# Optimization experiments

Measured on AMD Instinct MI355X. Metric: run time of the kernel, lower is better.

Reference implementation:

```python
import jax, jax.numpy as jnp
import numpy as np

# Fixed geometry from the module's voxel_dict
VOXEL = np.array([0.32, 0.32, 6.0], dtype=np.float32)
PC_MIN = np.array([-74.88, -74.88, -2.0], dtype=np.float32)
PC_MAX = np.array([74.88, 74.88, 4.0], dtype=np.float32)
NX, NY, NZ = 468, 468, 1          # round((max-min)/voxel) per axis
CANVAS = NZ * NY * NX             # 219024 voxels (batch_size = 1)
OFFSET = VOXEL / 2.0 + PC_MIN     # x/y/z_offset from __init__


def setup_inputs() -> dict:
    key = jax.random.key(0)
    k1, k2, k3, k4 = jax.random.split(key, 4)
    N = 400000
    # points uniformly inside the point-cloud range (dynamic voxelization keeps all)
    xyz = jax.random.uniform(k1, (N, 3), dtype=jnp.float32) * (PC_MAX - PC_MIN) * 0.999 + PC_MIN
    extra = jax.random.normal(k2, (N, 2), dtype=jnp.float32)
    points = jnp.concatenate([xyz, extra], axis=1)          # [N, 5]
    W1 = jax.random.normal(k3, (11, 64), dtype=jnp.float32) * 0.05
    W2 = jax.random.normal(k4, (128, 64), dtype=jnp.float32) * 0.05
    return {"points": points, "W1": W1, "W2": W2}


def _flat_voxel_index(xyz):
    # dynamic voxelization: integer voxel coord per point, (z, y, x) ordering
    c = jnp.floor((xyz - PC_MIN) / VOXEL).astype(jnp.int32)
    cx = jnp.clip(c[:, 0], 0, NX - 1)
    cy = jnp.clip(c[:, 1], 0, NY - 1)
    cz = jnp.clip(c[:, 2], 0, NZ - 1)
    flat = cz * (NY * NX) + cy * NX + cx                    # canvas index as in map_voxel_center_to_point
    return flat, cx, cy, cz


def reference(points, W1, W2):
    xyz = points[:, :3]
    flat, cx, cy, cz = _flat_voxel_index(xyz)

    # DynamicScatter mean (cluster_scatter)
    cnt = jax.ops.segment_sum(jnp.ones((points.shape[0],), jnp.float32), flat, num_segments=CANVAS)
    vsum = jax.ops.segment_sum(points, flat, num_segments=CANVAS)
    vmean = vsum / jnp.maximum(cnt, 1.0)[:, None]           # [CANVAS, 5]
    pmean = vmean[flat]                                     # gather voxel mean to points

    f_cluster = xyz - pmean[:, :3]
    centers = jnp.stack([cx, cy, cz], axis=1).astype(jnp.float32) * VOXEL + OFFSET
    f_center = xyz - centers
    features = jnp.concatenate([points, f_cluster, f_center], axis=-1)   # [N, 11]

    occ = (cnt > 0)[:, None]

    # PFN layer 1: Linear(bias=False) + ReLU, then scatter-max to voxels
    pf1 = jax.nn.relu(features @ W1)                        # [N, 64]
    v1 = jax.ops.segment_max(pf1, flat, num_segments=CANVAS)
    v1 = jnp.where(occ, v1, 0.0)                            # zero empty voxels (replaces -inf)

    # gather voxel max back to points, concat, PFN layer 2
    feat2 = jnp.concatenate([pf1, v1[flat]], axis=1)        # [N, 128]
    pf2 = jax.nn.relu(feat2 @ W2)                           # [N, 64]
    v2 = jax.ops.segment_max(pf2, flat, num_segments=CANVAS)
    v2 = jnp.where(occ, v2, 0.0)                            # [CANVAS, 64] dense voxel features
    return v2
```

## Files before the change

kernel.cpp:

```cpp
#include <hip/hip_runtime.h>

#define NXc 468
#define NYc 468
#define CANVASc (468 * 468)
#define NPTS 400000
#define RUN 16
#define NRUNS (NPTS / RUN)
#define GPTS ((NPTS + 255) / 256)
#define GVOX ((CANVASc + 255) / 256)
#define GSEAM ((NRUNS + 255) / 256)

#define PCMIN_X (-74.88f)
#define PCMIN_Y (-74.88f)
#define VOX_X 0.32f
#define VOX_Y 0.32f
#define OFF_X (-74.72f)
#define OFF_Y (-74.72f)
#define OFF_Z (1.0f)

typedef __attribute__((ext_vector_type(8))) short v8s;
typedef __attribute__((ext_vector_type(4))) float v4f;

static_assert(sizeof(__bf16) == 2, "bf16 must be 2 bytes");

__device__ __forceinline__ int rli(int x, int p) {
    return __builtin_amdgcn_readlane(x, p);
}

__device__ __forceinline__ void split8(const float* f, v8s& h, v8s& l) {
    #pragma unroll
    for (int i = 0; i < 8; i += 2) {
        __bf16 h0 = (__bf16)f[i];
        __bf16 h1 = (__bf16)f[i + 1];
        h[i]     = __builtin_bit_cast(short, h0);
        h[i + 1] = __builtin_bit_cast(short, h1);
        float l0 = f[i]     - (float)h0;
        float l1 = f[i + 1] - (float)h1;
        l[i]     = __builtin_bit_cast(short, (__bf16)l0);
        l[i + 1] = __builtin_bit_cast(short, (__bf16)l1);
    }
}

__device__ __forceinline__ int voxel_cell(float x, float y, int& cx, int& cy) {
    cx = (int)floorf((x - PCMIN_X) / VOX_X);
    cy = (int)floorf((y - PCMIN_Y) / VOX_Y);
    cx = min(max(cx, 0), NXc - 1);
    cy = min(max(cy, 0), NYc - 1);
    return cy * NXc + cx;
}

__device__ __forceinline__ void kw_body(int tid,
                                        const float* __restrict__ W1,
                                        const float* __restrict__ W2,
                                        v8s* __restrict__ w1frag,
                                        v8s* __restrict__ w2frag) {
    if (tid < 1024) {
        int f = tid >> 6, lane = tid & 63;
        int t = f >> 2, c = f & 3;
        int q = lane >> 4, n = lane & 15;
        float v[8];
        #pragma unroll
        for (int i = 0; i < 8; i++) v[i] = W2[(c * 32 + q * 8 + i) * 64 + t * 16 + n];
        v8s h, l;
        split8(v, h, l);
        w2frag[(f * 2 + 0) * 64 + lane] = h;
        w2frag[(f * 2 + 1) * 64 + lane] = l;
    } else if (tid < 1280) {
        int f = (tid - 1024) >> 6, lane = (tid - 1024) & 63;
        int q = lane >> 4, n = lane & 15;
        float v[8];
        #pragma unroll
        for (int i = 0; i < 8; i++) {
            int k = q * 8 + i;
            v[i] = (k < 11) ? W1[k * 64 + f * 16 + n] : 0.f;
        }
        v8s h, l;
        split8(v, h, l);
        w1frag[(f * 2 + 0) * 64 + lane] = h;
        w1frag[(f * 2 + 1) * 64 + lane] = l;
    }
}

__global__ __launch_bounds__(256) void k_stats(const float* __restrict__ pts,
                                               int* __restrict__ cnt,
                                               const float* __restrict__ W1,
                                               const float* __restrict__ W2,
                                               v8s* __restrict__ w1frag,
                                               v8s* __restrict__ w2frag) {
    int b = blockIdx.x;
    if (b >= GPTS) {
        kw_body((b - GPTS) * 256 + threadIdx.x, W1, W2, w1frag, w2frag);
        return;
    }
    int i = b * 256 + threadIdx.x;
    if (i >= NPTS) return;
    float x = pts[i * 5 + 0], y = pts[i * 5 + 1];
    int cx, cy;
    int fl = voxel_cell(x, y, cx, cy);
    atomicAdd(&cnt[fl], 1);
}

__global__ __launch_bounds__(256) void k_alloc(const int* __restrict__ cnt,
                                               int* __restrict__ cursor,
                                               int* __restrict__ gcur) {
    int v = blockIdx.x * 256 + threadIdx.x;
    int lane = threadIdx.x & 63;
    int c = (v < CANVASc) ? cnt[v] : 0;
    int scan = c;
    #pragma unroll
    for (int off = 1; off < 64; off <<= 1) {
        int t = __shfl_up(scan, off, 64);
        if (lane >= off) scan += t;
    }
    int total = __shfl(scan, 63, 64);
    int base = 0;
    if (lane == 0 && total > 0) base = atomicAdd(gcur, total);
    base = __shfl(base, 0, 64);
    if (v < CANVASc) cursor[v] = base + scan - c;
}

__device__ __forceinline__ void gather_pt(const float* __restrict__ pts, int pi,
                                          float4& A, float& e1) {
    const float* pp = pts + (size_t)pi * 5;
    __builtin_memcpy(&A, pp, 16);
    e1 = pp[4];
}

__global__ __launch_bounds__(256) void k_scatter(const float* __restrict__ pts,
                                                 int* __restrict__ cursor,
                                                 float4* __restrict__ pos4,
                                                 float* __restrict__ e1b,
                                                 int* __restrict__ cellb) {
    int i = blockIdx.x * 256 + threadIdx.x;
    if (i >= NPTS) return;
    float4 A; float e1;
    gather_pt(pts, i, A, e1);
    int cx, cy;
    int fl = voxel_cell(A.x, A.y, cx, cy);
    int pos = atomicAdd(&cursor[fl], 1);
    pos4[pos] = A;
    e1b[pos] = e1;
    cellb[pos] = cx | (cy << 16);
}

__global__ __launch_bounds__(256) void kV(const int* __restrict__ cnt,
                                          const int* __restrict__ cursor,
                                          const float4* __restrict__ pos4,
                                          const int* __restrict__ cellb,
                                          float4* __restrict__ vmean4,
                                          float4* __restrict__ v14,
                                          float4* __restrict__ out4) {
    int b = blockIdx.x;
    if (b >= GVOX) {
        int w = (b - GVOX) * 256 + threadIdx.x;
        if (w == 0 || w >= NRUNS) return;
        int bb = w * RUN;
        int ca = cellb[bb - 1], cb = cellb[bb];
        if (ca != cb) return;
        int cx = ca & 0xFFFF, cy = ca >> 16;
        int va = cy * NXc + cx;
        float4 z = make_float4(0.f, 0.f, 0.f, 0.f);
        float4* o = out4 + (size_t)va * 16;
        float4* q = v14 + (size_t)va * 16;
        #pragma unroll
        for (int i = 0; i < 16; i++) { o[i] = z; q[i] = z; }
        return;
    }
    int v = b * 256 + threadIdx.x;
    if (v >= CANVASc) return;
    int c = cnt[v];
    if (c == 0) {
        float4 z = make_float4(0.f, 0.f, 0.f, 0.f);
        float4* o = out4 + (size_t)v * 16;
        #pragma unroll
        for (int i = 0; i < 16; i++) o[i] = z;
        return;
    }
    int start = cursor[v] - c;
    float sx = 0.f, sy = 0.f, sz = 0.f;
    for (int i = 0; i < c; i++) {
        float4 p = pos4[start + i];
        sx += p.x; sy += p.y; sz += p.z;
    }
    float inv = 1.0f / (float)c;
    vmean4[v] = make_float4(sx * inv, sy * inv, sz * inv, 0.f);
}

struct PtRegs {
    float4 A;
    float  e1, fcx, fcy, fcz;
    float  mx, my, mz;
    int    vx;
};
__device__ __forceinline__ PtRegs load_pt(const float4* __restrict__ pos4,
                                          const float* __restrict__ e1b,
                                          const int* __restrict__ cellb,
                                          const float4* __restrict__ vmean4,
                                          int base, int j) {
    PtRegs r;
    r.A = make_float4(0.f, 0.f, 0.f, 0.f);
    r.e1 = r.fcx = r.fcy = r.fcz = r.mx = r.my = r.mz = 0.f;
    r.vx = -1;
    int idx = -1;
    if (j < RUN) idx = base + j;
    else if (j == 16) idx = (base + RUN < NPTS) ? base + RUN : -1;
    else if (j == 17) idx = base - 1;
    if (idx >= 0) {
        int cell = cellb[idx];
        int cx = cell & 0xFFFF, cy = cell >> 16;
        int vv = cy * NXc + cx;
        r.vx = vv;
        if (j < RUN) {
            float4 A = pos4[idx];
            r.A = A;
            r.e1 = e1b[idx];
            r.fcx = A.x - (cx * VOX_X + OFF_X);
            r.fcy = A.y - (cy * VOX_Y + OFF_Y);
            r.fcz = A.z - OFF_Z;
            float4 m = vmean4[vv];
            r.mx = m.x; r.my = m.y; r.mz = m.z;
        }
    }
    return r;
}

#define PSTR 68

__device__ __forceinline__ void phase1_mfma(float (*s_pf)[PSTR], const PtRegs& P,
                                            const v8s* __restrict__ w1frag, int j) {
    if (j < RUN) {
        float* row = s_pf[j];
        row[0] = P.A.x; row[1] = P.A.y; row[2] = P.A.z; row[3] = P.A.w; row[4] = P.e1;
        row[5] = P.A.x - P.mx; row[6] = P.A.y - P.my; row[7] = P.A.z - P.mz;
        row[8] = P.fcx; row[9] = P.fcy; row[10] = P.fcz;
        #pragma unroll
        for (int t = 11; t < 16; t++) row[t] = 0.f;
    }
    __builtin_amdgcn_wave_barrier();

    const int m = j & 15, q = j >> 4;
    v8s fh = {0,0,0,0,0,0,0,0}, fl_ = {0,0,0,0,0,0,0,0};
    if (q < 2) {
        float f8[8];
        #pragma unroll
        for (int i = 0; i < 8; i++) f8[i] = s_pf[m][q * 8 + i];
        split8(f8, fh, fl_);
    }
    v4f d[4];
    #pragma unroll
    for (int t = 0; t < 4; t++) {
        v8s bh = w1frag[(t * 2 + 0) * 64 + j];
        v8s bl = w1frag[(t * 2 + 1) * 64 + j];
        v4f acc = {0.f, 0.f, 0.f, 0.f};
        acc = __builtin_amdgcn_mfma_f32_16x16x32_bf16(fh,  bh, acc, 0, 0, 0);
        acc = __builtin_amdgcn_mfma_f32_16x16x32_bf16(fl_, bh, acc, 0, 0, 0);
        acc = __builtin_amdgcn_mfma_f32_16x16x32_bf16(fh,  bl, acc, 0, 0, 0);
        d[t] = acc;
    }
    __builtin_amdgcn_wave_barrier();
    #pragma unroll
    for (int t = 0; t < 4; t++)
        #pragma unroll
        for (int r = 0; r < 4; r++)
            s_pf[q * 4 + r][t * 16 + m] = fmaxf(d[t][r], 0.f);
    __builtin_amdgcn_wave_barrier();
}

__global__ __launch_bounds__(256) void kA(const float4* __restrict__ pos4,
                                          const float* __restrict__ e1b,
                                          const int* __restrict__ cellb,
                                          const float4* __restrict__ vmean4,
                                          const v8s* __restrict__ w1frag,
                                          float* __restrict__ v1) {
    __shared__ float s_pf[4][RUN][PSTR];
    int wslot = threadIdx.x >> 6;
    int wave = blockIdx.x * 4 + wslot;
    int j = threadIdx.x & 63;
    int base = wave * RUN;

    PtRegs P = load_pt(pos4, e1b, cellb, vmean4, base, j);

    const int first = rli(P.vx, 0), last = rli(P.vx, RUN - 1);
    const bool firstExt = (rli(P.vx, 17) == first);
    const bool lastExt  = (rli(P.vx, 16) == last);
    if (!firstExt && !lastExt) return;

    phase1_mfma(s_pf[wslot], P, w1frag, j);

    int vprev = first;
    float smax = 0.f;
    for (int p = 0; p < RUN; p++) {
        int vp = rli(P.vx, p);
        if (vp != vprev) {
            bool ua = (vprev == first && firstExt) || (vprev == last && lastExt);
            if (ua) atomicMax((int*)v1 + (size_t)vprev * 64 + j, __float_as_int(smax));
            vprev = vp; smax = 0.f;
        }
        smax = fmaxf(smax, s_pf[wslot][p][j]);
    }
    {
        bool ua = (vprev == first && firstExt) || (vprev == last && lastExt);
        if (ua) atomicMax((int*)v1 + (size_t)vprev * 64 + j, __float_as_int(smax));
    }
}

__global__ __launch_bounds__(256) void kB(const float4* __restrict__ pos4,
                                          const float* __restrict__ e1b,
                                          const int* __restrict__ cellb,
                                          const float4* __restrict__ vmean4,
                                          const v8s* __restrict__ w1frag,
                                          const v8s* __restrict__ w2frag,
                                          const float* __restrict__ v1,
                                          float* __restrict__ out) {
    __shared__ float s_pf[4][RUN][PSTR];
    int wslot = threadIdx.x >> 6;
    int wave = blockIdx.x * 4 + wslot;
    int j = threadIdx.x & 63;
    int base = wave * RUN;

    PtRegs P = load_pt(pos4, e1b, cellb, vmean4, base, j);

    const int m = j & 15, q = j >> 4;

    const int first = rli(P.vx, 0), last = rli(P.vx, RUN - 1);
    const bool firstExt = (rli(P.vx, 17) == first);
    const bool lastExt  = (rli(P.vx, 16) == last);

    int vx_m = __builtin_amdgcn_ds_bpermute(m << 2, P.vx);
    int vx_prev = __shfl_up(P.vx, 1, 64);
    unsigned long long B =
        __ballot((j < RUN) && ((j == 0) || (P.vx != vx_prev)));
    int s_seg = 63 - __builtin_clzll(B & ((2ULL << m) - 1ULL));
    int e_seg = m + 1 + (int)__builtin_ctzll((B | (1ULL << RUN)) >> (m + 1));
    const bool ext_m = (vx_m == first && firstExt) || (vx_m == last && lastExt);

    phase1_mfma(s_pf[wslot], P, w1frag, j);

    float vf[16];
    if (ext_m) {
        const float* vr = v1 + (size_t)vx_m * 64 + q * 8;
        #pragma unroll
        for (int c = 0; c < 2; c++)
            #pragma unroll
            for (int i = 0; i < 8; i++) vf[c * 8 + i] = vr[c * 32 + i];
    }

    v8s ah[4], al[4];
    #pragma unroll
    for (int c = 0; c < 2; c++) {
        float f[8];
        #pragma unroll
        for (int i = 0; i < 8; i++) f[i] = s_pf[wslot][m][c * 32 + q * 8 + i];
        split8(f, ah[c], al[c]);
    }
    if (!ext_m) {
        #pragma unroll
        for (int i = 0; i < 16; i++) vf[i] = 0.f;
        for (int p = s_seg; p < e_seg; p++) {
            const float* row = s_pf[wslot][p];
            float4 a0 = *(const float4*)&row[q * 8];
            float4 a1 = *(const float4*)&row[q * 8 + 4];
            float4 b0 = *(const float4*)&row[32 + q * 8];
            float4 b1 = *(const float4*)&row[32 + q * 8 + 4];
            vf[0] = fmaxf(vf[0], a0.x);  vf[1] = fmaxf(vf[1], a0.y);
            vf[2] = fmaxf(vf[2], a0.z);  vf[3] = fmaxf(vf[3], a0.w);
            vf[4] = fmaxf(vf[4], a1.x);  vf[5] = fmaxf(vf[5], a1.y);
            vf[6] = fmaxf(vf[6], a1.z);  vf[7] = fmaxf(vf[7], a1.w);
            vf[8] = fmaxf(vf[8], b0.x);  vf[9] = fmaxf(vf[9], b0.y);
            vf[10] = fmaxf(vf[10], b0.z); vf[11] = fmaxf(vf[11], b0.w);
            vf[12] = fmaxf(vf[12], b1.x); vf[13] = fmaxf(vf[13], b1.y);
            vf[14] = fmaxf(vf[14], b1.z); vf[15] = fmaxf(vf[15], b1.w);
        }
    }
    split8(vf + 0, ah[2], al[2]);
    split8(vf + 8, ah[3], al[3]);
    __builtin_amdgcn_wave_barrier();

    #pragma unroll
    for (int t = 0; t < 4; t++) {
        v8s bh[4], bl[4];
        #pragma unroll
        for (int c = 0; c < 4; c++) {
            bh[c] = w2frag[((t * 4 + c) * 2 + 0) * 64 + j];
            bl[c] = w2frag[((t * 4 + c) * 2 + 1) * 64 + j];
        }
        v4f acc = {0.f, 0.f, 0.f, 0.f};
        #pragma unroll
        for (int c = 0; c < 4; c++) {
            acc = __builtin_amdgcn_mfma_f32_16x16x32_bf16(ah[c], bh[c], acc, 0, 0, 0);
            acc = __builtin_amdgcn_mfma_f32_16x16x32_bf16(al[c], bh[c], acc, 0, 0, 0);
            acc = __builtin_amdgcn_mfma_f32_16x16x32_bf16(ah[c], bl[c], acc, 0, 0, 0);
        }
        #pragma unroll
        for (int r = 0; r < 4; r++) s_pf[wslot][q * 4 + r][t * 16 + m] = acc[r];
    }
    __builtin_amdgcn_wave_barrier();

    int vprev = first;
    float smax = -3.4e38f;
    for (int p = 0; p < RUN; p++) {
        int vp = rli(P.vx, p);
        if (vp != vprev) {
            float r = fmaxf(smax, 0.f);
            size_t o = (size_t)vprev * 64 + j;
            bool ua = (vprev == first && firstExt) || (vprev == last && lastExt);
            if (ua) atomicMax((int*)out + o, __float_as_int(r));
            else out[o] = r;
            vprev = vp; smax = -3.4e38f;
        }
        smax = fmaxf(smax, s_pf[wslot][p][j]);
    }
    {
        float r = fmaxf(smax, 0.f);
        size_t o = (size_t)vprev * 64 + j;
        bool ua = (vprev == first && firstExt) || (vprev == last && lastExt);
        if (ua) atomicMax((int*)out + o, __float_as_int(r));
        else out[o] = r;
    }
}

extern "C" void kernel_launch(void* const* d_in, const int* in_sizes, int n_in,
                              void* d_out, int out_size, void* d_ws, size_t ws_size,
                              hipStream_t stream) {
    const float* pts = (const float*)d_in[0];
    const float* W1  = (const float*)d_in[1];
    const float* W2  = (const float*)d_in[2];
    float* out = (float*)d_out;

    float4* vmean4 = (float4*)d_ws;
    float*  v1     = (float*)(vmean4 + CANVASc);
    float4* pos4   = (float4*)(v1 + (size_t)CANVASc * 64);
    float*  e1b    = (float*)(pos4 + NPTS);
    int*    cellb  = (int*)(e1b + NPTS);
    v8s*    w2frag = (v8s*)(cellb + NPTS);
    v8s*    w1frag = w2frag + 2048;
    int*    cnt    = (int*)(w1frag + 512);
    int*    gcur   = cnt + CANVASc;
    int*    cursor = gcur + 1;

    hipMemsetAsync(cnt, 0, (size_t)(CANVASc + 1) * 4, stream);

    k_stats  <<<GPTS + 5, 256, 0, stream>>>(pts, cnt, W1, W2, w1frag, w2frag);
    k_alloc  <<<GVOX, 256, 0, stream>>>(cnt, cursor, gcur);
    k_scatter<<<GPTS, 256, 0, stream>>>(pts, cursor, pos4, e1b, cellb);
    kV       <<<GVOX + GSEAM, 256, 0, stream>>>(cnt, cursor, pos4, cellb,
                                                vmean4, (float4*)v1, (float4*)out);
    kA       <<<NRUNS / 4, 256, 0, stream>>>(pos4, e1b, cellb, vmean4, w1frag, v1);
    kB       <<<NRUNS / 4, 256, 0, stream>>>(pos4, e1b, cellb, vmean4, w1frag,
                                             w2frag, v1, out);
}
```

Measured before the change: 236.6 us.

## Replace full-run kA pass with seam-voxel list and direct per-voxel max kernel

kA launched one wave per run of 16 points across all runs, recomputed phase-1 features with MFMA and used atomicMax for voxels spanning run boundaries. Now kV records seam voxels into a compacted list, and a new kAL kernel with a fixed grid walks only those voxels. For each one it computes the layer-1 max directly with scalar FMAs over the voxel's points and writes it without atomics. This removes the zeroing of v1 for seam voxels, the atomics and the wasted waves that exited early. In exchange it adds a global atomic counter and uses fp32 FMAs instead of the split-bf16 MFMA, which can change rounding slightly.

```diff
diff --git a/kernel.cpp b/kernel.cpp
--- a/kernel.cpp
+++ b/kernel.cpp
@@ -25,6 +25,9 @@
 
 __device__ __forceinline__ int rli(int x, int p) {
     return __builtin_amdgcn_readlane(x, p);
+}
+__device__ __forceinline__ float rlf(float x, int p) {
+    return __int_as_float(__builtin_amdgcn_readlane(__float_as_int(x), p));
 }
 
 __device__ __forceinline__ void split8(const float* f, v8s& h, v8s& l) {
@@ -148,8 +151,9 @@
                                           const float4* __restrict__ pos4,
                                           const int* __restrict__ cellb,
                                           float4* __restrict__ vmean4,
-                                          float4* __restrict__ v14,
-                                          float4* __restrict__ out4) {
+                                          float4* __restrict__ out4,
+                                          int* __restrict__ scnt,
+                                          int* __restrict__ slist) {
     int b = blockIdx.x;
     if (b >= GVOX) {
         int w = (b - GVOX) * 256 + threadIdx.x;
@@ -159,11 +163,12 @@
         if (ca != cb) return;
         int cx = ca & 0xFFFF, cy = ca >> 16;
         int va = cy * NXc + cx;
+        int pos = atomicAdd(scnt, 1);
+        slist[pos] = va;
         float4 z = make_float4(0.f, 0.f, 0.f, 0.f);
         float4* o = out4 + (size_t)va * 16;
-        float4* q = v14 + (size_t)va * 16;
-        #pragma unroll
-        for (int i = 0; i < 16; i++) { o[i] = z; q[i] = z; }
+        #pragma unroll
+        for (int i = 0; i < 16; i++) o[i] = z;
         return;
     }
     int v = b * 256 + threadIdx.x;
@@ -184,6 +189,57 @@
     }
     float inv = 1.0f / (float)c;
     vmean4[v] = make_float4(sx * inv, sy * inv, sz * inv, 0.f);
+}
+
+__global__ __launch_bounds__(256) void kAL(const int* __restrict__ scnt,
+                                           const int* __restrict__ slist,
+                                           const int* __restrict__ cnt,
+                                           const int* __restrict__ cursor,
+                                           const float4* __restrict__ pos4,
+                                           const float* __restrict__ e1b,
+                                           const int* __restrict__ cellb,
+                                           const float4* __restrict__ vmean4,
+                                           const float* __restrict__ W1,
+                                           float* __restrict__ v1) {
+    int j = threadIdx.x & 63;
+    int wslot = threadIdx.x >> 6;
+    int nseam = scnt[0];
+    float w[11];
+    #pragma unroll
+    for (int k = 0; k < 11; k++) w[k] = W1[k * 64 + j];
+    for (int s = blockIdx.x * 4 + wslot; s < nseam; s += gridDim.x * 4) {
+        int v = slist[s];
+        int c = cnt[v];
+        int start = cursor[v] - c;
+        float vmax = 0.f;
+        for (int pb = 0; pb < c; pb += 64) {
+            int pc = min(c - pb, 64);
+            float f[11];
+            #pragma unroll
+            for (int k = 0; k < 11; k++) f[k] = 0.f;
+            if (j < pc) {
+                int idx = start + pb + j;
+                float4 A = pos4[idx];
+                float e1 = e1b[idx];
+                int cell = cellb[idx];
+                int cx = cell & 0xFFFF, cy = cell >> 16;
+                float4 mv = vmean4[v];
+                f[0] = A.x; f[1] = A.y; f[2] = A.z; f[3] = A.w; f[4] = e1;
+                f[5] = A.x - mv.x; f[6] = A.y - mv.y; f[7] = A.z - mv.z;
+                f[8] = A.x - (cx * VOX_X + OFF_X);
+                f[9] = A.y - (cy * VOX_Y + OFF_Y);
+                f[10] = A.z - OFF_Z;
+            }
+            for (int p = 0; p < pc; p++) {
+                float acc = 0.f;
+                #pragma unroll
+                for (int k = 0; k < 11; k++)
+                    acc = fmaf(rlf(f[k], p), w[k], acc);
+                vmax = fmaxf(vmax, acc);
+            }
+        }
+        v1[(size_t)v * 64 + j] = vmax;
+    }
 }
 
 struct PtRegs {
@@ -266,44 +322,6 @@
     __builtin_amdgcn_wave_barrier();
 }
 
-__global__ __launch_bounds__(256) void kA(const float4* __restrict__ pos4,
-                                          const float* __restrict__ e1b,
-                                          const int* __restrict__ cellb,
-                                          const float4* __restrict__ vmean4,
-                                          const v8s* __restrict__ w1frag,
-                                          float* __restrict__ v1) {
-    __shared__ float s_pf[4][RUN][PSTR];
-    int wslot = threadIdx.x >> 6;
-    int wave = blockIdx.x * 4 + wslot;
-    int j = threadIdx.x & 63;
-    int base = wave * RUN;
-
-    PtRegs P = load_pt(pos4, e1b, cellb, vmean4, base, j);
-
-    const int first = rli(P.vx, 0), last = rli(P.vx, RUN - 1);
-    const bool firstExt = (rli(P.vx, 17) == first);
-    const bool lastExt  = (rli(P.vx, 16) == last);
-    if (!firstExt && !lastExt) return;
-
-    phase1_mfma(s_pf[wslot], P, w1frag, j);
-
-    int vprev = first;
-    float smax = 0.f;
-    for (int p = 0; p < RUN; p++) {
-        int vp = rli(P.vx, p);
-        if (vp != vprev) {
-            bool ua = (vprev == first && firstExt) || (vprev == last && lastExt);
-            if (ua) atomicMax((int*)v1 + (size_t)vprev * 64 + j, __float_as_int(smax));
-            vprev = vp; smax = 0.f;
-        }
-        smax = fmaxf(smax, s_pf[wslot][p][j]);
-    }
-    {
-        bool ua = (vprev == first && firstExt) || (vprev == last && lastExt);
-        if (ua) atomicMax((int*)v1 + (size_t)vprev * 64 + j, __float_as_int(smax));
-    }
-}
-
 __global__ __launch_bounds__(256) void kB(const float4* __restrict__ pos4,
                                           const float* __restrict__ e1b,
                                           const int* __restrict__ cellb,
@@ -436,16 +454,19 @@
     v8s*    w1frag = w2frag + 2048;
     int*    cnt    = (int*)(w1frag + 512);
     int*    gcur   = cnt + CANVASc;
-    int*    cursor = gcur + 1;
-
-    hipMemsetAsync(cnt, 0, (size_t)(CANVASc + 1) * 4, stream);
+    int*    scnt   = gcur + 1;
+    int*    slist  = scnt + 1;
+    int*    cursor = slist + NRUNS;
+
+    hipMemsetAsync(cnt, 0, (size_t)(CANVASc + 2) * 4, stream);
 
     k_stats  <<<GPTS + 5, 256, 0, stream>>>(pts, cnt, W1, W2, w1frag, w2frag);
     k_alloc  <<<GVOX, 256, 0, stream>>>(cnt, cursor, gcur);
     k_scatter<<<GPTS, 256, 0, stream>>>(pts, cursor, pos4, e1b, cellb);
     kV       <<<GVOX + GSEAM, 256, 0, stream>>>(cnt, cursor, pos4, cellb,
-                                                vmean4, (float4*)v1, (float4*)out);
-    kA       <<<NRUNS / 4, 256, 0, stream>>>(pos4, e1b, cellb, vmean4, w1frag, v1);
+                                                vmean4, (float4*)out, scnt, slist);
+    kAL      <<<256, 256, 0, stream>>>(scnt, slist, cnt, cursor, pos4, e1b,
+                                       cellb, vmean4, W1, v1);
     kB       <<<NRUNS / 4, 256, 0, stream>>>(pos4, e1b, cellb, vmean4, w1frag,
                                              w2frag, v1, out);
 }
```

Measured after the change: 251.4 us. +6.3%, slower.
